# Kernel optimization log

Measured on AMD Instinct MI355X. Metric: run time of the kernel, lower is better.

Reference implementation:

```python
import jax, jax.numpy as jnp
import numpy as np

EPS = 1e-5

def _bilinear_sample(xb, ys, xs):
    # xb: [C,H,W]; ys, xs: [H,W] float sample coordinates (zero outside bounds)
    C, H, W = xb.shape
    y0 = jnp.floor(ys); x0 = jnp.floor(xs)
    y1 = y0 + 1.0;      x1 = x0 + 1.0
    wy1 = ys - y0; wy0 = 1.0 - wy1
    wx1 = xs - x0; wx0 = 1.0 - wx1
    def g(yi, xi):
        valid = (yi >= 0) & (yi < H) & (xi >= 0) & (xi < W)
        yc = jnp.clip(yi, 0, H - 1).astype(jnp.int32)
        xc = jnp.clip(xi, 0, W - 1).astype(jnp.int32)
        return xb[:, yc, xc] * valid[None].astype(xb.dtype)  # [C,H,W]
    return (g(y0, x0) * (wy0 * wx0)[None] + g(y0, x1) * (wy0 * wx1)[None]
          + g(y1, x0) * (wy1 * wx0)[None] + g(y1, x1) * (wy1 * wx1)[None])

def _deform_conv2d(x, offset, mask, w, b):
    # x:[B,C,H,W] offset:[B,18,H,W] mask:[B,9,H,W] w:[Co,C,3,3] b:[Co]
    B, C, H, W = x.shape
    Co = w.shape[0]
    ii = jnp.arange(H, dtype=x.dtype)[:, None]
    jj = jnp.arange(W, dtype=x.dtype)[None, :]
    cols = []
    for k in range(9):  # fixed 3x3 kernel positions, row-major (dy=offset[2k], dx=offset[2k+1])
        ky, kx = k // 3 - 1, k % 3 - 1
        ys = ii + ky + offset[:, 2 * k]      # [B,H,W]
        xs = jj + kx + offset[:, 2 * k + 1]
        v = jax.vmap(_bilinear_sample)(x, ys, xs)  # [B,C,H,W]
        cols.append(v * mask[:, k][:, None])
    cols = jnp.stack(cols, axis=1)               # [B,9,C,H,W]
    out = jnp.einsum('bkchw,ock->bohw', cols, w.reshape(Co, C, 9))
    return out + b[None, :, None, None]

def setup_inputs() -> dict:
    key = jax.random.key(0)
    k1, k2, k3, k4 = jax.random.split(key, 4)
    B, Cin, Cout, H, W = 8, 64, 64, 128, 128
    x = jax.random.normal(k1, (B, Cin, H, W), dtype=jnp.float32)
    # offset/mask conv: small weights so learned offsets stay O(1) pixels;
    # bias[18:]=2.0 as in the module's init (masks start near sigmoid(2))
    w_off = jax.random.normal(k2, (27, Cin, 3, 3), dtype=jnp.float32) * 0.01
    b_off = jnp.concatenate([jnp.zeros((18,), jnp.float32), jnp.full((9,), 2.0, jnp.float32)])
    w_dcn = jax.random.normal(k3, (Cout, Cin, 3, 3), dtype=jnp.float32) / np.sqrt(Cin * 9)
    b_dcn = jax.random.normal(k4, (Cout,), dtype=jnp.float32) * 0.01
    return {"x": x, "w_off": w_off, "b_off": b_off, "w_dcn": w_dcn, "b_dcn": b_dcn}

def reference(x, w_off, b_off, w_dcn, b_dcn):
    dn = ('NCHW', 'OIHW', 'NCHW')
    om = jax.lax.conv_general_dilated(x, w_off, (1, 1), 'SAME', dimension_numbers=dn)
    om = om + b_off[None, :, None, None]
    offset = om[:, :18]
    mask = jax.nn.sigmoid(om[:, 18:])
    y = _deform_conv2d(x, offset, mask, w_dcn, b_dcn)
    # InstanceNorm2d (affine=False, biased variance) + ReLU
    mu = jnp.mean(y, axis=(2, 3), keepdims=True)
    var = jnp.var(y, axis=(2, 3), keepdims=True)
    y = (y - mu) * jax.lax.rsqrt(var + EPS)
    return jax.nn.relu(y)
```

## Files before the change

kernel.cpp:

```cpp
#include <hip/hip_runtime.h>
#include <hip/hip_bf16.h>

#define BB   8
#define CIN  64
#define COUT 64
#define HH   128
#define WW   128
#define HWSZ (HH * WW)

typedef short bf16x8 __attribute__((ext_vector_type(8)));
typedef float f32x4  __attribute__((ext_vector_type(4)));
typedef float f32x2  __attribute__((ext_vector_type(2)));

__device__ __forceinline__ unsigned f2bf_u(float f) {
    unsigned u = __float_as_uint(f);
    return (u + 0x7fffu + ((u >> 16) & 1u)) >> 16;
}

__device__ __forceinline__ unsigned comb2(unsigned a, unsigned b, unsigned c, unsigned d,
                                          f32x2 W0, f32x2 W1, f32x2 W2, f32x2 W3) {
    f32x2 A = {__uint_as_float(a << 16), __uint_as_float(a & 0xffff0000u)};
    f32x2 B = {__uint_as_float(b << 16), __uint_as_float(b & 0xffff0000u)};
    f32x2 C = {__uint_as_float(c << 16), __uint_as_float(c & 0xffff0000u)};
    f32x2 D = {__uint_as_float(d << 16), __uint_as_float(d & 0xffff0000u)};
    f32x2 r = A * W0;
    r += B * W1;
    r += C * W2;
    r += D * W3;
    __hip_bfloat162 h = __float22bfloat162_rn(make_float2(r.x, r.y));
    return *(const unsigned*)&h;
}

__global__ __launch_bounds__(256) void k_tr(const float* __restrict__ x,
                                            unsigned short* __restrict__ xT)
{
    __shared__ unsigned short tile[256 * 66];
    const int t = threadIdx.x;
    const int b = blockIdx.y;
    const int p0 = blockIdx.x * 256;
#pragma unroll
    for (int i = 0; i < 16; ++i) {
        int c = i * 4 + (t >> 6);
        int pl = (t & 63) * 4;
        float4 v = *(const float4*)(x + (((size_t)b * 64 + c) << 14) + p0 + pl);
        tile[(pl + 0) * 66 + c] = (unsigned short)f2bf_u(v.x);
        tile[(pl + 1) * 66 + c] = (unsigned short)f2bf_u(v.y);
        tile[(pl + 2) * 66 + c] = (unsigned short)f2bf_u(v.z);
        tile[(pl + 3) * 66 + c] = (unsigned short)f2bf_u(v.w);
    }
    __syncthreads();
#pragma unroll
    for (int i = 0; i < 8; ++i) {
        int id = i * 256 + t;
        int pt = id >> 3, ck = id & 7;
        const unsigned* srcp = (const unsigned*)&tile[pt * 66 + ck * 8];
        uint4 r;
        r.x = srcp[0]; r.y = srcp[1]; r.z = srcp[2]; r.w = srcp[3];
        *(uint4*)(xT + ((size_t)b << 20) + (size_t)(p0 + pt) * 64 + ck * 8) = r;
    }
}

__global__ __launch_bounds__(256) void k_wcvt(const float* __restrict__ wd,
                                              const float* __restrict__ wof,
                                              unsigned short* __restrict__ wdT,
                                              unsigned short* __restrict__ wofT)
{
    int idx = blockIdx.x * 256 + threadIdx.x;
    if (idx < 36864) {
        int k = idx >> 12, rem = idx & 4095, co = rem >> 6, c = rem & 63;
        wdT[idx] = (unsigned short)f2bf_u(wd[(co * 64 + c) * 9 + k]);
    } else {
        int j = idx - 36864;
        int k = j >> 11, rem = j & 2047, o = rem >> 6, c = rem & 63;
        wofT[j] = (o < 27) ? (unsigned short)f2bf_u(wof[(o * 64 + c) * 9 + k]) : 0;
    }
}

__global__ __launch_bounds__(256, 2) void k_off(
    const unsigned short* __restrict__ xT, const unsigned short* __restrict__ wofT,
    const float* __restrict__ bof, float* __restrict__ om)
{
    __shared__ unsigned short tile[8 * 521 * 8];
    const int t = threadIdx.x;
    const int lane = t & 63, wv = t >> 6;
    const int q = lane >> 4, l15 = lane & 15;
    const int b = blockIdx.y;
    const int h0 = blockIdx.x * 2;
    const int r0 = h0 - 1;
    const unsigned short* xb = xT + ((size_t)b << 20);

#pragma unroll
    for (int i = 0; i < 17; ++i) {
        int id = i * 256 + t;
        if (id < 4160) {
            int m = id & 7, lin = id >> 3;
            int row = lin / 130, col = lin % 130;
            int gy = r0 + row, gx = col - 1;
            uint4 v = {0u, 0u, 0u, 0u};
            if (((unsigned)gy < (unsigned)HH) && ((unsigned)gx < (unsigned)WW))
                v = *(const uint4*)(xb + ((size_t)(gy * WW + gx) << 6) + m * 8);
            *(uint4*)&tile[(m * 521 + lin) * 8] = v;
        }
    }
    __syncthreads();

    const int hrow = h0 + (wv >> 1);
    const int c0 = (wv & 1) * 64;

    f32x4 acc[2][4];
#pragma unroll
    for (int mt = 0; mt < 2; ++mt)
#pragma unroll
        for (int nt = 0; nt < 4; ++nt) acc[mt][nt] = (f32x4){0.f, 0.f, 0.f, 0.f};

#pragma unroll
    for (int k = 0; k < 9; ++k) {
        const int ky = k / 3 - 1, kx = k % 3 - 1;
        const int trow = (hrow - h0) + ky + 1;
        const unsigned short* wk = wofT + k * 2048;
#pragma unroll
        for (int ks = 0; ks < 2; ++ks) {
            bf16x8 af[2], bfr[4];
#pragma unroll
            for (int mt = 0; mt < 2; ++mt)
                af[mt] = *(const bf16x8*)(wk + (mt * 16 + l15) * 64 + ks * 32 + q * 8);
#pragma unroll
            for (int nt = 0; nt < 4; ++nt) {
                int tc = c0 + nt * 16 + l15 + kx + 1;
                bfr[nt] = *(const bf16x8*)&tile[((ks * 4 + q) * 521 + trow * 130 + tc) * 8];
            }
#pragma unroll
            for (int mt = 0; mt < 2; ++mt)
#pragma unroll
                for (int nt = 0; nt < 4; ++nt)
                    acc[mt][nt] = __builtin_amdgcn_mfma_f32_16x16x32_bf16(
                        af[mt], bfr[nt], acc[mt][nt], 0, 0, 0);
        }
    }

    const int p0 = blockIdx.x * 256 + wv * 64;
    float* omb = om + (size_t)b * 27 * HWSZ;
#pragma unroll
    for (int mt = 0; mt < 2; ++mt)
#pragma unroll
        for (int r = 0; r < 4; ++r) {
            int o = mt * 16 + q * 4 + r;
            if (o < 27) {
                float bias = bof[o];
#pragma unroll
                for (int nt = 0; nt < 4; ++nt) {
                    int pp = p0 + nt * 16 + l15;
                    float v = acc[mt][nt][r] + bias;
                    if (o >= 18) v = 1.f / (1.f + __expf(-v));
                    omb[(size_t)o * HWSZ + pp] = v;
                }
            }
        }
}

__global__ __launch_bounds__(256, 2) void k_dcn(
    const unsigned short* __restrict__ xT, const float* __restrict__ om,
    const unsigned short* __restrict__ wdT, const float* __restrict__ bd,
    float* __restrict__ out, float2* __restrict__ sums)
{
    __shared__ unsigned short col_sh[4][64 * 80];
    __shared__ unsigned       adr_sh[4][4][64];
    __shared__ float4         w_sh[4][64];
    __shared__ float          redS[4][64];
    __shared__ float          redQ[4][64];

    const int t = threadIdx.x;
    const int lane = t & 63, wv = t >> 6;
    const int q = lane >> 4, l15 = lane & 15;
    const int pblk = blockIdx.x * 256;
    const int p = pblk + t;
    const int b = blockIdx.y;
    const int h = p >> 7, w = p & 127;
    const char* xbB = (const char*)(xT + ((size_t)b << 20));
    const float* omp = om + (size_t)b * 27 * HWSZ + p;
    const int gck = lane & 7;

    f32x4 acc[4][4];
#pragma unroll
    for (int mt = 0; mt < 4; ++mt)
#pragma unroll
        for (int nt = 0; nt < 4; ++nt) acc[mt][nt] = (f32x4){0.f, 0.f, 0.f, 0.f};

#define LOADG(P, g) { \
    int pt_ = (g) * 8 + (lane >> 3); \
    unsigned o0_ = adr_sh[wv][0][pt_]; \
    unsigned o1_ = adr_sh[wv][1][pt_]; \
    unsigned o2_ = adr_sh[wv][2][pt_]; \
    unsigned o3_ = adr_sh[wv][3][pt_]; \
    int bo_ = gck * 16; \
    P[0] = *(const uint4*)(xbB + o0_ + bo_); \
    P[1] = *(const uint4*)(xbB + o1_ + bo_); \
    P[2] = *(const uint4*)(xbB + o2_ + bo_); \
    P[3] = *(const uint4*)(xbB + o3_ + bo_); }

#define COMBG(P, g) { \
    int pt_ = (g) * 8 + (lane >> 3); \
    float4 w4_ = w_sh[wv][pt_]; \
    f32x2 W0_ = {w4_.x, w4_.x}, W1_ = {w4_.y, w4_.y}; \
    f32x2 W2_ = {w4_.z, w4_.z}, W3_ = {w4_.w, w4_.w}; \
    uint4 R_; \
    R_.x = comb2(P[0].x, P[1].x, P[2].x, P[3].x, W0_, W1_, W2_, W3_); \
    R_.y = comb2(P[0].y, P[1].y, P[2].y, P[3].y, W0_, W1_, W2_, W3_); \
    R_.z = comb2(P[0].z, P[1].z, P[2].z, P[3].z, W0_, W1_, W2_, W3_); \
    R_.w = comb2(P[0].w, P[1].w, P[2].w, P[3].w, W0_, W1_, W2_, W3_); \
    *(uint4*)&col_sh[wv][pt_ * 80 + gck * 8] = R_; }

    float offy = omp[0];
    float offx = omp[HWSZ];
    float mk   = omp[18 * HWSZ];

    for (int k = 0; k < 9; ++k) {
        float ys = (float)(h + (k / 3) - 1) + offy;
        float xs = (float)(w + (k % 3) - 1) + offx;
        float fy0 = floorf(ys), fx0 = floorf(xs);
        float wy1 = ys - fy0, wx1 = xs - fx0;
        float wy0 = 1.f - wy1, wx0 = 1.f - wx1;
        int y0 = (int)fy0, x0 = (int)fx0;
        int y1 = y0 + 1, x1 = x0 + 1;
        bool vy0 = (y0 >= 0) && (y0 < HH), vy1 = (y1 >= 0) && (y1 < HH);
        bool vx0 = (x0 >= 0) && (x0 < WW), vx1 = (x1 >= 0) && (x1 < WW);
        int y0c = min(max(y0, 0), HH - 1), y1c = min(max(y1, 0), HH - 1);
        int x0c = min(max(x0, 0), WW - 1), x1c = min(max(x1, 0), WW - 1);
        adr_sh[wv][0][lane] = (unsigned)((y0c * WW + x0c) << 7);
        adr_sh[wv][1][lane] = (unsigned)((y0c * WW + x1c) << 7);
        adr_sh[wv][2][lane] = (unsigned)((y1c * WW + x0c) << 7);
        adr_sh[wv][3][lane] = (unsigned)((y1c * WW + x1c) << 7);
        w_sh[wv][lane] = make_float4((vy0 && vx0) ? mk * wy0 * wx0 : 0.f,
                                     (vy0 && vx1) ? mk * wy0 * wx1 : 0.f,
                                     (vy1 && vx0) ? mk * wy1 * wx0 : 0.f,
                                     (vy1 && vx1) ? mk * wy1 * wx1 : 0.f);
        int kn = (k < 8) ? k + 1 : 8;
        offy = omp[(2 * kn) * HWSZ];
        offx = omp[(2 * kn + 1) * HWSZ];
        mk   = omp[(18 + kn) * HWSZ];
        __builtin_amdgcn_wave_barrier();

        const unsigned short* wk = wdT + k * 4096;
        bf16x8 af[2][4];
#pragma unroll
        for (int ks = 0; ks < 2; ++ks)
#pragma unroll
            for (int mt = 0; mt < 4; ++mt)
                af[ks][mt] = *(const bf16x8*)(wk + (mt * 16 + l15) * 64 + ks * 32 + q * 8);

        uint4 pb[3][4];
        LOADG(pb[0], 0);
        LOADG(pb[1], 1);
#pragma unroll
        for (int g = 0; g < 8; ++g) {
            if (g + 2 < 8) LOADG(pb[(g + 2) % 3], g + 2);
            COMBG(pb[g % 3], g);
        }
        __builtin_amdgcn_wave_barrier();

#pragma unroll
        for (int ks = 0; ks < 2; ++ks) {
            bf16x8 bfr[4];
#pragma unroll
            for (int nt = 0; nt < 4; ++nt)
                bfr[nt] = *(const bf16x8*)&col_sh[wv][(nt * 16 + l15) * 80 + ks * 32 + q * 8];
#pragma unroll
            for (int mt = 0; mt < 4; ++mt)
#pragma unroll
                for (int nt = 0; nt < 4; ++nt)
                    acc[mt][nt] = __builtin_amdgcn_mfma_f32_16x16x32_bf16(
                        af[ks][mt], bfr[nt], acc[mt][nt], 0, 0, 0);
        }
    }
#undef LOADG
#undef COMBG

    const int p0 = pblk + wv * 64;
    float* outb = out + (size_t)b * COUT * HWSZ;
#pragma unroll
    for (int mt = 0; mt < 4; ++mt)
#pragma unroll
        for (int r = 0; r < 4; ++r) {
            int co = mt * 16 + q * 4 + r;
            float bias = bd[co];
            float s = 0.f, qq = 0.f;
#pragma unroll
            for (int nt = 0; nt < 4; ++nt) {
                float v = acc[mt][nt][r] + bias;
                outb[(size_t)co * HWSZ + p0 + nt * 16 + l15] = v;
                s += v; qq += v * v;
            }
#pragma unroll
            for (int m = 1; m < 16; m <<= 1) {
                s += __shfl_xor(s, m);
                qq += __shfl_xor(qq, m);
            }
            if (l15 == 0) { redS[wv][co] = s; redQ[wv][co] = qq; }
        }
    __syncthreads();
    if (t < 64) {
        float S = redS[0][t] + redS[1][t] + redS[2][t] + redS[3][t];
        float Q = redQ[0][t] + redQ[1][t] + redQ[2][t] + redQ[3][t];
        atomicAdd(&sums[b * 64 + t].x, S);
        atomicAdd(&sums[b * 64 + t].y, Q);
    }
}

__global__ __launch_bounds__(256) void k_norm(float* __restrict__ out,
                                              const float2* __restrict__ sums)
{
    const int i = blockIdx.x * 256 + threadIdx.x;
    const int bco = i >> 12;
    float2 sq = sums[bco];
    float mu  = sq.x * (1.f / (float)HWSZ);
    float var = sq.y * (1.f / (float)HWSZ) - mu * mu;
    float rstd = rsqrtf(var + 1e-5f);
    float4* o4 = (float4*)out;
    float4 v = o4[i];
    v.x = fmaxf((v.x - mu) * rstd, 0.f);
    v.y = fmaxf((v.y - mu) * rstd, 0.f);
    v.z = fmaxf((v.z - mu) * rstd, 0.f);
    v.w = fmaxf((v.w - mu) * rstd, 0.f);
    o4[i] = v;
}

extern "C" void kernel_launch(void* const* d_in, const int* in_sizes, int n_in,
                              void* d_out, int out_size, void* d_ws, size_t ws_size,
                              hipStream_t stream) {
    const float* x   = (const float*)d_in[0];
    const float* wof = (const float*)d_in[1];
    const float* bof = (const float*)d_in[2];
    const float* wd  = (const float*)d_in[3];
    const float* bd  = (const float*)d_in[4];
    float* out = (float*)d_out;

    char* ws = (char*)d_ws;
    unsigned short* xT   = (unsigned short*)ws;
    float*          om   = (float*)(ws + 16777216);
    unsigned short* wdT  = (unsigned short*)(ws + 30932992);
    unsigned short* wofT = (unsigned short*)(ws + 31006720);
    float2*         sums = (float2*)(ws + 31043584);

    hipMemsetAsync(sums, 0, 4096, stream);
    k_tr    <<<dim3(64, 8), 256, 0, stream>>>(x, xT);
    k_wcvt  <<<216, 256, 0, stream>>>(wd, wof, wdT, wofT);
    k_off   <<<dim3(64, 8), 256, 0, stream>>>(xT, wofT, bof, om);
    k_dcn   <<<dim3(64, 8), 256, 0, stream>>>(xT, om, wdT, bd, out, sums);
    k_norm  <<<8192, 256, 0, stream>>>(out, (const float2*)sums);
}
```

Measured before the change: 173.1 us.

## Halve k_dcn per-wave pixel tile to raise occupancy; fold weight cast into transpose

```diff
diff --git a/kernel.cpp b/kernel.cpp
--- a/kernel.cpp
+++ b/kernel.cpp
@@ -32,10 +32,30 @@
 }
 
 __global__ __launch_bounds__(256) void k_tr(const float* __restrict__ x,
-                                            unsigned short* __restrict__ xT)
+                                            const float* __restrict__ wd,
+                                            const float* __restrict__ wof,
+                                            unsigned short* __restrict__ xT,
+                                            unsigned short* __restrict__ wdT,
+                                            unsigned short* __restrict__ wofT)
 {
+    const int t = threadIdx.x;
+    if (blockIdx.y == 8) {
+        int base = blockIdx.x * 256 + t;
+#pragma unroll
+        for (int j = 0; j < 4; ++j) {
+            int idx = base + j * 16384;
+            if (idx < 36864) {
+                int k = idx >> 12, rem = idx & 4095, co = rem >> 6, c = rem & 63;
+                wdT[idx] = (unsigned short)f2bf_u(wd[(co * 64 + c) * 9 + k]);
+            } else if (idx < 55296) {
+                int jj = idx - 36864;
+                int k = jj >> 11, rem = jj & 2047, o = rem >> 6, c = rem & 63;
+                wofT[jj] = (o < 27) ? (unsigned short)f2bf_u(wof[(o * 64 + c) * 9 + k]) : 0;
+            }
+        }
+        return;
+    }
     __shared__ unsigned short tile[256 * 66];
-    const int t = threadIdx.x;
     const int b = blockIdx.y;
     const int p0 = blockIdx.x * 256;
 #pragma unroll
@@ -57,22 +77,6 @@
         uint4 r;
         r.x = srcp[0]; r.y = srcp[1]; r.z = srcp[2]; r.w = srcp[3];
         *(uint4*)(xT + ((size_t)b << 20) + (size_t)(p0 + pt) * 64 + ck * 8) = r;
-    }
-}
-
-__global__ __launch_bounds__(256) void k_wcvt(const float* __restrict__ wd,
-                                              const float* __restrict__ wof,
-                                              unsigned short* __restrict__ wdT,
-                                              unsigned short* __restrict__ wofT)
-{
-    int idx = blockIdx.x * 256 + threadIdx.x;
-    if (idx < 36864) {
-        int k = idx >> 12, rem = idx & 4095, co = rem >> 6, c = rem & 63;
-        wdT[idx] = (unsigned short)f2bf_u(wd[(co * 64 + c) * 9 + k]);
-    } else {
-        int j = idx - 36864;
-        int k = j >> 11, rem = j & 2047, o = rem >> 6, c = rem & 63;
-        wofT[j] = (o < 27) ? (unsigned short)f2bf_u(wof[(o * 64 + c) * 9 + k]) : 0;
     }
 }
 
@@ -158,33 +162,33 @@
         }
 }
 
-__global__ __launch_bounds__(256, 2) void k_dcn(
+__global__ __launch_bounds__(256, 4) void k_dcn(
     const unsigned short* __restrict__ xT, const float* __restrict__ om,
     const unsigned short* __restrict__ wdT, const float* __restrict__ bd,
     float* __restrict__ out, float2* __restrict__ sums)
 {
-    __shared__ unsigned short col_sh[4][64 * 80];
-    __shared__ unsigned       adr_sh[4][4][64];
-    __shared__ float4         w_sh[4][64];
+    __shared__ unsigned short col_sh[4][32 * 80];
+    __shared__ unsigned       adr_sh[4][4][32];
+    __shared__ float4         w_sh[4][32];
     __shared__ float          redS[4][64];
     __shared__ float          redQ[4][64];
 
     const int t = threadIdx.x;
     const int lane = t & 63, wv = t >> 6;
     const int q = lane >> 4, l15 = lane & 15;
-    const int pblk = blockIdx.x * 256;
-    const int p = pblk + t;
     const int b = blockIdx.y;
-    const int h = p >> 7, w = p & 127;
+    const int wp0 = blockIdx.x * 128 + wv * 32;
+    const int myp = wp0 + (lane & 31);
+    const int h = myp >> 7, w = myp & 127;
     const char* xbB = (const char*)(xT + ((size_t)b << 20));
-    const float* omp = om + (size_t)b * 27 * HWSZ + p;
+    const float* omp = om + (size_t)b * 27 * HWSZ + myp;
     const int gck = lane & 7;
 
-    f32x4 acc[4][4];
+    f32x4 acc[4][2];
 #pragma unroll
     for (int mt = 0; mt < 4; ++mt)
 #pragma unroll
-        for (int nt = 0; nt < 4; ++nt) acc[mt][nt] = (f32x4){0.f, 0.f, 0.f, 0.f};
+        for (int nt = 0; nt < 2; ++nt) acc[mt][nt] = (f32x4){0.f, 0.f, 0.f, 0.f};
 
 #define LOADG(P, g) { \
     int pt_ = (g) * 8 + (lane >> 3); \
@@ -210,34 +214,40 @@
     R_.w = comb2(P[0].w, P[1].w, P[2].w, P[3].w, W0_, W1_, W2_, W3_); \
     *(uint4*)&col_sh[wv][pt_ * 80 + gck * 8] = R_; }
 
-    float offy = omp[0];
-    float offx = omp[HWSZ];
-    float mk   = omp[18 * HWSZ];
+    float offy = 0.f, offx = 0.f, mk = 0.f;
+    if (lane < 32) {
+        offy = omp[0];
+        offx = omp[HWSZ];
+        mk   = omp[18 * HWSZ];
+    }
 
     for (int k = 0; k < 9; ++k) {
-        float ys = (float)(h + (k / 3) - 1) + offy;
-        float xs = (float)(w + (k % 3) - 1) + offx;
-        float fy0 = floorf(ys), fx0 = floorf(xs);
-        float wy1 = ys - fy0, wx1 = xs - fx0;
-        float wy0 = 1.f - wy1, wx0 = 1.f - wx1;
-        int y0 = (int)fy0, x0 = (int)fx0;
-        int y1 = y0 + 1, x1 = x0 + 1;
-        bool vy0 = (y0 >= 0) && (y0 < HH), vy1 = (y1 >= 0) && (y1 < HH);
-        bool vx0 = (x0 >= 0) && (x0 < WW), vx1 = (x1 >= 0) && (x1 < WW);
-        int y0c = min(max(y0, 0), HH - 1), y1c = min(max(y1, 0), HH - 1);
-        int x0c = min(max(x0, 0), WW - 1), x1c = min(max(x1, 0), WW - 1);
-        adr_sh[wv][0][lane] = (unsigned)((y0c * WW + x0c) << 7);
-        adr_sh[wv][1][lane] = (unsigned)((y0c * WW + x1c) << 7);
-        adr_sh[wv][2][lane] = (unsigned)((y1c * WW + x0c) << 7);
-        adr_sh[wv][3][lane] = (unsigned)((y1c * WW + x1c) << 7);
-        w_sh[wv][lane] = make_float4((vy0 && vx0) ? mk * wy0 * wx0 : 0.f,
-                                     (vy0 && vx1) ? mk * wy0 * wx1 : 0.f,
-                                     (vy1 && vx0) ? mk * wy1 * wx0 : 0.f,
-                                     (vy1 && vx1) ? mk * wy1 * wx1 : 0.f);
-        int kn = (k < 8) ? k + 1 : 8;
-        offy = omp[(2 * kn) * HWSZ];
-        offx = omp[(2 * kn + 1) * HWSZ];
-        mk   = omp[(18 + kn) * HWSZ];
+        if (lane < 32) {
+            float ys = (float)(h + (k / 3) - 1) + offy;
+            float xs = (float)(w + (k % 3) - 1) + offx;
+            float fy0 = floorf(ys), fx0 = floorf(xs);
+            float wy1 = ys - fy0, wx1 = xs - fx0;
+            float wy0 = 1.f - wy1, wx0 = 1.f - wx1;
+            int y0 = (int)fy0, x0 = (int)fx0;
+            int y1 = y0 + 1, x1 = x0 + 1;
+            bool vy0 = (y0 >= 0) && (y0 < HH), vy1 = (y1 >= 0) && (y1 < HH);
+            bool vx0 = (x0 >= 0) && (x0 < WW), vx1 = (x1 >= 0) && (x1 < WW);
+            int y0c = min(max(y0, 0), HH - 1), y1c = min(max(y1, 0), HH - 1);
+            int x0c = min(max(x0, 0), WW - 1), x1c = min(max(x1, 0), WW - 1);
+            int pl = lane & 31;
+            adr_sh[wv][0][pl] = (unsigned)((y0c * WW + x0c) << 7);
+            adr_sh[wv][1][pl] = (unsigned)((y0c * WW + x1c) << 7);
+            adr_sh[wv][2][pl] = (unsigned)((y1c * WW + x0c) << 7);
+            adr_sh[wv][3][pl] = (unsigned)((y1c * WW + x1c) << 7);
+            w_sh[wv][pl] = make_float4((vy0 && vx0) ? mk * wy0 * wx0 : 0.f,
+                                       (vy0 && vx1) ? mk * wy0 * wx1 : 0.f,
+                                       (vy1 && vx0) ? mk * wy1 * wx0 : 0.f,
+                                       (vy1 && vx1) ? mk * wy1 * wx1 : 0.f);
+            int kn = (k < 8) ? k + 1 : 8;
+            offy = omp[(2 * kn) * HWSZ];
+            offx = omp[(2 * kn + 1) * HWSZ];
+            mk   = omp[(18 + kn) * HWSZ];
+        }
         __builtin_amdgcn_wave_barrier();
 
         const unsigned short* wk = wdT + k * 4096;
@@ -252,22 +262,22 @@
         LOADG(pb[0], 0);
         LOADG(pb[1], 1);
 #pragma unroll
-        for (int g = 0; g < 8; ++g) {
-            if (g + 2 < 8) LOADG(pb[(g + 2) % 3], g + 2);
+        for (int g = 0; g < 4; ++g) {
+            if (g + 2 < 4) LOADG(pb[(g + 2) % 3], g + 2);
             COMBG(pb[g % 3], g);
         }
         __builtin_amdgcn_wave_barrier();
 
 #pragma unroll
         for (int ks = 0; ks < 2; ++ks) {
-            bf16x8 bfr[4];
-#pragma unroll
-            for (int nt = 0; nt < 4; ++nt)
+            bf16x8 bfr[2];
+#pragma unroll
+            for (int nt = 0; nt < 2; ++nt)
                 bfr[nt] = *(const bf16x8*)&col_sh[wv][(nt * 16 + l15) * 80 + ks * 32 + q * 8];
 #pragma unroll
             for (int mt = 0; mt < 4; ++mt)
 #pragma unroll
-                for (int nt = 0; nt < 4; ++nt)
+                for (int nt = 0; nt < 2; ++nt)
                     acc[mt][nt] = __builtin_amdgcn_mfma_f32_16x16x32_bf16(
                         af[ks][mt], bfr[nt], acc[mt][nt], 0, 0, 0);
         }
@@ -275,7 +285,6 @@
 #undef LOADG
 #undef COMBG
 
-    const int p0 = pblk + wv * 64;
     float* outb = out + (size_t)b * COUT * HWSZ;
 #pragma unroll
     for (int mt = 0; mt < 4; ++mt)
@@ -285,9 +294,9 @@
             float bias = bd[co];
             float s = 0.f, qq = 0.f;
 #pragma unroll
-            for (int nt = 0; nt < 4; ++nt) {
+            for (int nt = 0; nt < 2; ++nt) {
                 float v = acc[mt][nt][r] + bias;
-                outb[(size_t)co * HWSZ + p0 + nt * 16 + l15] = v;
+                outb[(size_t)co * HWSZ + wp0 + nt * 16 + l15] = v;
                 s += v; qq += v * v;
             }
 #pragma unroll
@@ -342,9 +351,8 @@
     float2*         sums = (float2*)(ws + 31043584);
 
     hipMemsetAsync(sums, 0, 4096, stream);
-    k_tr    <<<dim3(64, 8), 256, 0, stream>>>(x, xT);
-    k_wcvt  <<<216, 256, 0, stream>>>(wd, wof, wdT, wofT);
+    k_tr    <<<dim3(64, 9), 256, 0, stream>>>(x, wd, wof, xT, wdT, wofT);
     k_off   <<<dim3(64, 8), 256, 0, stream>>>(xT, wofT, bof, om);
-    k_dcn   <<<dim3(64, 8), 256, 0, stream>>>(xT, om, wdT, bd, out, sums);
+    k_dcn   <<<dim3(128, 8), 256, 0, stream>>>(xT, om, wdT, bd, out, sums);
     k_norm  <<<8192, 256, 0, stream>>>(out, (const float2*)sums);
 }
```

After: 188.7 us. 1.09x slower.
